# Kernel optimization log

Measured on AMD Instinct MI355X. Metric: run time of the kernel, lower is better.

Reference implementation:

```python
import jax, jax.numpy as jnp
import numpy as np

B, I, S, H, O = 128, 64, 2048, 128, 64


def setup_inputs() -> dict:
    key = jax.random.key(0)
    ks = jax.random.split(key, 9)
    sc = 0.1
    return {
        "x": jax.random.normal(ks[0], (B, I, S), dtype=jnp.float32),
        "Wx_out": jax.random.normal(ks[1], (I, 4 * H), dtype=jnp.float32) * sc,
        "Wh_out": jax.random.normal(ks[2], (H, 4 * H), dtype=jnp.float32) * sc,
        "b_out": jnp.zeros((4 * H,), dtype=jnp.float32),
        "Wx_in": jax.random.normal(ks[3], (H, 4 * H), dtype=jnp.float32) * sc,
        "Wh_in": jax.random.normal(ks[4], (H, 4 * H), dtype=jnp.float32) * sc,
        "b_in": jnp.zeros((4 * H,), dtype=jnp.float32),
        "W_lin": jax.random.normal(ks[5], (O, H), dtype=jnp.float32) * 0.01,
        "b_lin": jnp.zeros((O,), dtype=jnp.float32),
    }


def reference(x, Wx_out, Wh_out, b_out, Wx_in, Wh_in, b_in, W_lin, b_lin):
    # x: (B, I, S) -> permute(0,2,1) -> (B, S, I); scan over time axis.
    xs = jnp.transpose(x, (2, 0, 1))  # (S, B, I)
    h0 = jnp.zeros((x.shape[0], Wh_out.shape[0]), dtype=x.dtype)

    def step(carry, xt):
        h, c, cn = carry  # outer hidden, outer cell, inner cell
        gates = xt @ Wx_out + h @ Wh_out + b_out
        i, f, o, g = jnp.split(gates, 4, axis=-1)
        i, f, o = jax.nn.sigmoid(i), jax.nn.sigmoid(f), jax.nn.sigmoid(o)
        g = jnp.tanh(g)
        x_in = i * g          # inner LSTM input
        h_in = f * c          # inner LSTM hidden
        gi = x_in @ Wx_in + h_in @ Wh_in + b_in
        ii, fi, oi, gg = jnp.split(gi, 4, axis=-1)
        cn_new = jax.nn.sigmoid(fi) * cn + jax.nn.sigmoid(ii) * jnp.tanh(gg)
        c_new = jax.nn.sigmoid(oi) * jnp.tanh(cn_new)  # outer cell = inner hidden
        h_new = o * jnp.tanh(c_new)
        return (h_new, c_new, cn_new), h_new

    _, hs = jax.lax.scan(step, (h0, h0, h0), xs)  # hs: (S, B, H)
    hs = jnp.transpose(hs, (1, 0, 2))             # (B, S, H)
    return hs @ W_lin.T + b_lin                   # (B, S, O)
```

## Files before the change

kernel.cpp:

```cpp
#include <hip/hip_runtime.h>
#include <hip/hip_fp16.h>

#define BB 128
#define II 64
#define SS 2048
#define HH 128
#define GG 512
#define OO 64

typedef _Float16 f16x2 __attribute__((ext_vector_type(2)));
union F4H { float4 f4; f16x2 h[4]; };

__device__ __forceinline__ f16x2 pack2(float a, float b) {
    f16x2 r; r.x = (_Float16)a; r.y = (_Float16)b; return r;
}

__device__ __forceinline__ float dot2(f16x2 w, f16x2 v, float c) {
#if __has_builtin(__builtin_amdgcn_fdot2)
    return __builtin_amdgcn_fdot2(w, v, c, false);
#else
    return fmaf((float)w.x, (float)v.x, fmaf((float)w.y, (float)v.y, c));
#endif
}

__device__ __forceinline__ float tanh_f(float v) {
    float a = fabsf(v);
    float e = __expf(-2.0f * a);
    float r = (1.0f - e) * __builtin_amdgcn_rcpf(1.0f + e);
    return v < 0.0f ? -r : r;
}

template<int P>
__device__ __forceinline__ float qp(float v) {
    return __int_as_float(__builtin_amdgcn_mov_dpp(
        __float_as_int(v), P, 0xF, 0xF, true));
}
template<int C>
__device__ __forceinline__ float qb(float v) { return qp<0x55 * C>(v); }
template<int N>
__device__ __forceinline__ float rolN(float v) {
    return __int_as_float(__builtin_amdgcn_mov_dpp(
        __float_as_int(v), 0x120 + (16 - N), 0xF, 0xF, true));
}

__device__ __forceinline__ void barrier_lds() {
    asm volatile("s_waitcnt lgkmcnt(0)\n\ts_barrier" ::: "memory");
}

__global__ void __launch_bounds__(512)
nlstm_gatex(const float* __restrict__ x, const float* __restrict__ Wx_out,
            const float* __restrict__ b_out, float* __restrict__ gx,
            int t0, int nchunk)
{
    const int bb  = blockIdx.x / nchunk;
    const int tcw = blockIdx.x % nchunk;
    const int j   = threadIdx.x;
    const int u = j >> 2, g = j & 3;
    const int jcol = g * HH + u;

    __shared__ __align__(16) f16x2 xs[128][36];

    f16x2 wxo[II / 2];
#pragma unroll
    for (int m = 0; m < II / 2; ++m)
        wxo[m] = pack2(Wx_out[(2 * m) * GG + jcol],
                       Wx_out[(2 * m + 1) * GG + jcol]);
    const float bo = b_out[jcol];

    const float* xrow = x + (size_t)bb * II * SS;
    const int T0 = t0 + tcw * 128;
#pragma unroll
    for (int r = 0; r < 8; ++r) {
        const int idx = r * 512 + j;
        const int m = idx >> 7, tt = idx & 127;
        xs[tt][m] = pack2(xrow[(size_t)(2 * m) * SS + T0 + tt],
                          xrow[(size_t)(2 * m + 1) * SS + T0 + tt]);
    }
    __syncthreads();

#pragma unroll 1
    for (int tt = 0; tt < 128; ++tt) {
        const float4* xc4 = (const float4*)&xs[tt][0];
        float a0 = bo, a1 = 0.f, a2 = 0.f, a3 = 0.f;
#pragma unroll
        for (int c = 0; c < 8; ++c) {
            F4H xu; xu.f4 = xc4[c];
            a0 = dot2(wxo[4 * c + 0], xu.h[0], a0);
            a1 = dot2(wxo[4 * c + 1], xu.h[1], a1);
            a2 = dot2(wxo[4 * c + 2], xu.h[2], a2);
            a3 = dot2(wxo[4 * c + 3], xu.h[3], a3);
        }
        const float v = (a0 + a1) + (a2 + a3);
        const size_t tl = (size_t)tcw * 128 + tt;
        gx[((size_t)bb * nchunk * 128 + tl) * GG + j] = v;
    }
}

template<bool PROJ_IN>
__global__ void __launch_bounds__(512)
__attribute__((amdgpu_waves_per_eu(2)))
nlstm_scan_seg(
    const float* __restrict__ Wh_out,
    const float* __restrict__ Wx_in, const float* __restrict__ Wh_in,
    const float* __restrict__ b_in,
    const float* __restrict__ W_lin, const float* __restrict__ b_lin,
    const float* __restrict__ gx, float* __restrict__ out,
    f16x2* __restrict__ hws, f16x2* __restrict__ hst,
    float* __restrict__ cst, float* __restrict__ cnst,
    int t0, int t1, int Tc)
{
    const int b = blockIdx.x;
    const int j = threadIdx.x;
    const int u = j >> 2;
    const int g = j & 3;
    const int jcol = g * HH + u;

    __shared__ __align__(16) f16x2 hb[HH / 2];
    __shared__ __align__(16) f16x2 xib[HH / 2];
    __shared__ __align__(16) f16x2 hib[HH / 2];

    f16x2 who[4][16];
    f16x2 wxi[4][16];
    f16x2 whi[4][16];
#pragma unroll
    for (int c = 0; c < 4; ++c)
#pragma unroll
        for (int c4 = 0; c4 < 4; ++c4)
#pragma unroll
            for (int e = 0; e < 4; ++e) {
                const int k0 = 8 * (g + 4 * c4) + 2 * e;
                const int cc = c * HH + u;
                who[c][4 * c4 + e] = pack2(Wh_out[(size_t)k0 * GG + cc],
                                           Wh_out[(size_t)(k0 + 1) * GG + cc]);
                wxi[c][4 * c4 + e] = pack2(Wx_in[(size_t)k0 * GG + cc],
                                           Wx_in[(size_t)(k0 + 1) * GG + cc]);
                whi[c][4 * c4 + e] = pack2(Wh_in[(size_t)k0 * GG + cc],
                                           Wh_in[(size_t)(k0 + 1) * GG + cc]);
            }

    const float bi2 = b_in[jcol];

    const int   pn = j >> 3;
    const int   ps = j & 7;
    float bl = 0.f;
    F4H wl[2];
    if constexpr (PROJ_IN) {
        bl = b_lin[pn];
#pragma unroll
        for (int q = 0; q < 2; ++q) {
            const int c = 2 * ps + q;
#pragma unroll
            for (int r = 0; r < 4; ++r)
                wl[q].h[r] = pack2(W_lin[pn * HH + 8 * c + 2 * r],
                                   W_lin[pn * HH + 8 * c + 2 * r + 1]);
        }
    }

    float* orow = out + (size_t)b * SS * OO;
    f16x2* hrow = (PROJ_IN ? (f16x2*)nullptr : hws + (size_t)b * SS * (HH / 2));
    const float* gxrow = gx + (size_t)b * Tc * GG;

    float c_reg, cn_reg;
    if (t0 == 0) {
        if (j < HH / 2) hb[j] = pack2(0.f, 0.f);
        c_reg = 0.f; cn_reg = 0.f;
    } else {
        if (j < HH / 2) hb[j] = hst[b * (HH / 2) + j];
        c_reg  = cst[b * HH + u];
        cn_reg = cnst[b * HH + u];
    }
    __syncthreads();

    const float4* hb4 = (const float4*)hb;
    const float4* xi4 = (const float4*)xib;
    const float4* hi4 = (const float4*)hib;
    const bool isT = (g == 3);

    float gx_cur = gxrow[j];

#pragma unroll 1
    for (int t = t0; t < t1; ++t) {
        const int tl = t - t0;

        const int tln = (tl + 1 < Tc) ? tl + 1 : tl;
        const float gx_nxt = gxrow[(size_t)tln * GG + j];

        float p0 = 0.f, p1 = 0.f, p2 = 0.f, p3 = 0.f;
#pragma unroll
        for (int c4 = 0; c4 < 4; ++c4) {
            F4H hu; hu.f4 = hb4[g + 4 * c4];
#pragma unroll
            for (int e = 0; e < 4; ++e) {
                p0 = dot2(who[0][4 * c4 + e], hu.h[e], p0);
                p1 = dot2(who[1][4 * c4 + e], hu.h[e], p1);
                p2 = dot2(who[2][4 * c4 + e], hu.h[e], p2);
                p3 = dot2(who[3][4 * c4 + e], hu.h[e], p3);
            }
        }
        p0 += qp<0xB1>(p0); p1 += qp<0xB1>(p1);
        p2 += qp<0xB1>(p2); p3 += qp<0xB1>(p3);
        p0 += qp<0x4E>(p0); p1 += qp<0x4E>(p1);
        p2 += qp<0x4E>(p2); p3 += qp<0x4E>(p3);
        const float totO = (g & 1) ? ((g & 2) ? p3 : p1)
                                   : ((g & 2) ? p2 : p0);
        float acc = totO + gx_cur;

        float ap = isT ? 2.f * acc : acc;
        float s  = __builtin_amdgcn_rcpf(1.f + __expf(-ap));
        float av = isT ? fmaf(2.f, s, -1.f) : s;

        float vi = qb<0>(av), vf = qb<1>(av), vo = qb<2>(av), vg = qb<3>(av);
        float x_in    = vi * vg;
        float h_in    = vf * c_reg;
        float o_outer = vo;

        if constexpr (PROJ_IN) {
            float q0 = 0.f, q1 = 0.f;
            F4H hu0; hu0.f4 = hb4[2 * ps];
            F4H hu1; hu1.f4 = hb4[2 * ps + 1];
            q0 = dot2(wl[0].h[0], hu0.h[0], q0);
            q1 = dot2(wl[0].h[1], hu0.h[1], q1);
            q0 = dot2(wl[0].h[2], hu0.h[2], q0);
            q1 = dot2(wl[0].h[3], hu0.h[3], q1);
            q0 = dot2(wl[1].h[0], hu1.h[0], q0);
            q1 = dot2(wl[1].h[1], hu1.h[1], q1);
            q0 = dot2(wl[1].h[2], hu1.h[2], q0);
            q1 = dot2(wl[1].h[3], hu1.h[3], q1);
            float p = q0 + q1;
            p += rolN<4>(p);
            p += rolN<2>(p);
            p += rolN<1>(p);
            if (ps == 0 && t > 0) orow[(size_t)(t - 1) * OO + pn] = p + bl;
        }

        float xin_n = rolN<4>(x_in);
        float hin_n = rolN<4>(h_in);
        if ((j & 7) == 0) {
            xib[u >> 1] = pack2(x_in, xin_n);
            hib[u >> 1] = pack2(h_in, hin_n);
        }
        barrier_lds();

        float s0 = 0.f, s1 = 0.f, s2 = 0.f, s3 = 0.f;
#pragma unroll
        for (int c4 = 0; c4 < 4; ++c4) {
            F4H xu; xu.f4 = xi4[g + 4 * c4];
#pragma unroll
            for (int e = 0; e < 4; ++e) {
                s0 = dot2(wxi[0][4 * c4 + e], xu.h[e], s0);
                s1 = dot2(wxi[1][4 * c4 + e], xu.h[e], s1);
                s2 = dot2(wxi[2][4 * c4 + e], xu.h[e], s2);
                s3 = dot2(wxi[3][4 * c4 + e], xu.h[e], s3);
            }
        }
#pragma unroll
        for (int c4 = 0; c4 < 4; ++c4) {
            F4H hu2; hu2.f4 = hi4[g + 4 * c4];
#pragma unroll
            for (int e = 0; e < 4; ++e) {
                s0 = dot2(whi[0][4 * c4 + e], hu2.h[e], s0);
                s1 = dot2(whi[1][4 * c4 + e], hu2.h[e], s1);
                s2 = dot2(whi[2][4 * c4 + e], hu2.h[e], s2);
                s3 = dot2(whi[3][4 * c4 + e], hu2.h[e], s3);
            }
        }
        s0 += qp<0xB1>(s0); s1 += qp<0xB1>(s1);
        s2 += qp<0xB1>(s2); s3 += qp<0xB1>(s3);
        s0 += qp<0x4E>(s0); s1 += qp<0x4E>(s1);
        s2 += qp<0x4E>(s2); s3 += qp<0x4E>(s3);
        const float totI = (g & 1) ? ((g & 2) ? s3 : s1)
                                   : ((g & 2) ? s2 : s0);
        float acc2 = totI + bi2;

        float ap2 = isT ? 2.f * acc2 : acc2;
        float s2a = __builtin_amdgcn_rcpf(1.f + __expf(-ap2));
        float av2 = isT ? fmaf(2.f, s2a, -1.f) : s2a;

        float ii = qb<0>(av2), fi = qb<1>(av2), oi = qb<2>(av2), gg = qb<3>(av2);
        float cn_new = fmaf(fi, cn_reg, ii * gg);
        cn_reg = cn_new;
        float c_new = oi * tanh_f(cn_new);
        c_reg = c_new;
        float h_new = o_outer * tanh_f(c_new);

        float hn_n = rolN<4>(h_new);
        if ((j & 7) == 0) {
            f16x2 hp = pack2(h_new, hn_n);
            hb[u >> 1] = hp;
            if constexpr (!PROJ_IN)
                hrow[(size_t)t * (HH / 2) + (j >> 3)] = hp;
        }
        gx_cur = gx_nxt;
        barrier_lds();
    }

    if (j < HH / 2) hst[b * (HH / 2) + j] = hb[j];
    if (g == 0) { cst[b * HH + u] = c_reg; cnst[b * HH + u] = cn_reg; }

    if constexpr (PROJ_IN) {
        if (t1 == SS) {
            float q0 = 0.f, q1 = 0.f;
            F4H hu0; hu0.f4 = hb4[2 * ps];
            F4H hu1; hu1.f4 = hb4[2 * ps + 1];
            q0 = dot2(wl[0].h[0], hu0.h[0], q0);
            q1 = dot2(wl[0].h[1], hu0.h[1], q1);
            q0 = dot2(wl[0].h[2], hu0.h[2], q0);
            q1 = dot2(wl[0].h[3], hu0.h[3], q1);
            q0 = dot2(wl[1].h[0], hu1.h[0], q0);
            q1 = dot2(wl[1].h[1], hu1.h[1], q1);
            q0 = dot2(wl[1].h[2], hu1.h[2], q0);
            q1 = dot2(wl[1].h[3], hu1.h[3], q1);
            float p = q0 + q1;
            p += rolN<4>(p);
            p += rolN<2>(p);
            p += rolN<1>(p);
            if (ps == 0) orow[(size_t)(SS - 1) * OO + pn] = p + bl;
        }
    }
}

__global__ void __launch_bounds__(512)
__attribute__((amdgpu_waves_per_eu(2)))
nlstm_fused(
    const float* __restrict__ x,
    const float* __restrict__ Wx_out, const float* __restrict__ Wh_out,
    const float* __restrict__ b_out,
    const float* __restrict__ Wx_in, const float* __restrict__ Wh_in,
    const float* __restrict__ b_in,
    const float* __restrict__ W_lin, const float* __restrict__ b_lin,
    float* __restrict__ out)
{
    const int b = blockIdx.x;
    const int j = threadIdx.x;
    const int u = j >> 2, g = j & 3;
    const int jcol = g * HH + u;

    __shared__ __align__(16) float4 wxf[8 * 512];
    __shared__ __align__(16) f16x2 xt[2][16][36];
    __shared__ __align__(16) f16x2 hb[HH / 2];
    __shared__ __align__(16) f16x2 xib[HH / 2];
    __shared__ __align__(16) f16x2 hib[HH / 2];

    f16x2 who[HH / 2], wxi[HH / 2], whi[HH / 2];
#pragma unroll
    for (int m = 0; m < HH / 2; ++m)
        who[m] = pack2(Wh_out[(2 * m) * GG + jcol], Wh_out[(2 * m + 1) * GG + jcol]);
#pragma unroll
    for (int m = 0; m < HH / 2; ++m)
        wxi[m] = pack2(Wx_in[(2 * m) * GG + jcol], Wx_in[(2 * m + 1) * GG + jcol]);
#pragma unroll
    for (int m = 0; m < HH / 2; ++m)
        whi[m] = pack2(Wh_in[(2 * m) * GG + jcol], Wh_in[(2 * m + 1) * GG + jcol]);

    const float bo = b_out[jcol];
    const float bi2 = b_in[jcol];
    const int pn = j >> 3, ps = j & 7;
    const float bl = b_lin[pn];
    F4H wl[2];
#pragma unroll
    for (int q = 0; q < 2; ++q) {
        const int c = 2 * ps + q;
#pragma unroll
        for (int r = 0; r < 4; ++r)
            wl[q].h[r] = pack2(W_lin[pn * HH + 8 * c + 2 * r],
                               W_lin[pn * HH + 8 * c + 2 * r + 1]);
    }
#pragma unroll
    for (int c = 0; c < 8; ++c) {
        F4H w4;
#pragma unroll
        for (int q = 0; q < 4; ++q)
            w4.h[q] = pack2(Wx_out[(8 * c + 2 * q) * GG + jcol],
                            Wx_out[(8 * c + 2 * q + 1) * GG + jcol]);
        wxf[c * 512 + j] = w4.f4;
    }

    const float* xrow = x + (size_t)b * II * SS;
    float* orow = out + (size_t)b * SS * OO;
    const int xm = j >> 4, xtl = j & 15;
    const float* xg0 = xrow + (size_t)(2 * xm) * SS + xtl;
    const float* xg1 = xrow + (size_t)(2 * xm + 1) * SS + xtl;

    xt[0][xtl][xm] = pack2(xg0[0], xg1[0]);
    if (j < HH / 2) hb[j] = pack2(0.f, 0.f);
    __syncthreads();

    float c_reg = 0.f, cn_reg = 0.f;
    const float4* hb4 = (const float4*)hb;
    const float4* xi4 = (const float4*)xib;
    const float4* hi4 = (const float4*)hib;
    const bool isT = (g == 3);
    float pr0 = 0.f, pr1 = 0.f;

#pragma unroll 1
    for (int t = 0; t < SS; ++t) {
        const int stl = t & 15;
        const int tb = (t >> 4) & 1;
        if (stl == 0) {
            const int Tn = (t + 16 < SS) ? t + 16 : t;
            pr0 = xg0[Tn];
            pr1 = xg1[Tn];
        }
        const float4* xc4 = (const float4*)&xt[tb][stl][0];
        float a0 = bo, a1 = 0.f, a2 = 0.f, a3 = 0.f;
#pragma unroll
        for (int c = 0; c < 8; ++c) {
            F4H xu; xu.f4 = xc4[c];
            F4H wu; wu.f4 = wxf[c * 512 + j];
            a0 = dot2(wu.h[0], xu.h[0], a0);
            a1 = dot2(wu.h[1], xu.h[1], a1);
            a2 = dot2(wu.h[2], xu.h[2], a2);
            a3 = dot2(wu.h[3], xu.h[3], a3);
        }
#pragma unroll
        for (int c = 0; c < 16; ++c) {
            F4H hu; hu.f4 = hb4[c];
            a0 = dot2(who[4 * c + 0], hu.h[0], a0);
            a1 = dot2(who[4 * c + 1], hu.h[1], a1);
            a2 = dot2(who[4 * c + 2], hu.h[2], a2);
            a3 = dot2(who[4 * c + 3], hu.h[3], a3);
        }
        float acc = (a0 + a1) + (a2 + a3);
        float ap = isT ? 2.f * acc : acc;
        float s = __builtin_amdgcn_rcpf(1.f + __expf(-ap));
        float av = isT ? fmaf(2.f, s, -1.f) : s;
        float vi = qb<0>(av), vf = qb<1>(av), vo = qb<2>(av), vg = qb<3>(av);
        float x_in = vi * vg, h_in = vf * c_reg, o_outer = vo;

        float p0 = 0.f, p1 = 0.f;
        {
            F4H hu0; hu0.f4 = hb4[2 * ps];
            F4H hu1; hu1.f4 = hb4[2 * ps + 1];
            p0 = dot2(wl[0].h[0], hu0.h[0], p0);
            p1 = dot2(wl[0].h[1], hu0.h[1], p1);
            p0 = dot2(wl[0].h[2], hu0.h[2], p0);
            p1 = dot2(wl[0].h[3], hu0.h[3], p1);
            p0 = dot2(wl[1].h[0], hu1.h[0], p0);
            p1 = dot2(wl[1].h[1], hu1.h[1], p1);
            p0 = dot2(wl[1].h[2], hu1.h[2], p0);
            p1 = dot2(wl[1].h[3], hu1.h[3], p1);
        }
        float p = p0 + p1;
        p += rolN<4>(p);
        p += rolN<2>(p);
        p += rolN<1>(p);
        if (ps == 0 && t > 0) orow[(size_t)(t - 1) * OO + pn] = p + bl;

        float xin_n = rolN<4>(x_in);
        float hin_n = rolN<4>(h_in);
        if ((j & 7) == 0) {
            xib[u >> 1] = pack2(x_in, xin_n);
            hib[u >> 1] = pack2(h_in, hin_n);
        }
        barrier_lds();

        float b0 = 0.f, b1 = 0.f, b2 = 0.f, b3 = 0.f;
#pragma unroll
        for (int c = 0; c < 16; ++c) {
            F4H xu; xu.f4 = xi4[c];
            b0 = dot2(wxi[4 * c + 0], xu.h[0], b0);
            b1 = dot2(wxi[4 * c + 1], xu.h[1], b1);
            b2 = dot2(wxi[4 * c + 2], xu.h[2], b2);
            b3 = dot2(wxi[4 * c + 3], xu.h[3], b3);
        }
#pragma unroll
        for (int c = 0; c < 16; ++c) {
            F4H hu; hu.f4 = hi4[c];
            b0 = dot2(whi[4 * c + 0], hu.h[0], b0);
            b1 = dot2(whi[4 * c + 1], hu.h[1], b1);
            b2 = dot2(whi[4 * c + 2], hu.h[2], b2);
            b3 = dot2(whi[4 * c + 3], hu.h[3], b3);
        }
        float acc2 = ((b0 + b1) + (b2 + b3)) + bi2;
        float ap2 = isT ? 2.f * acc2 : acc2;
        float s2 = __builtin_amdgcn_rcpf(1.f + __expf(-ap2));
        float av2 = isT ? fmaf(2.f, s2, -1.f) : s2;
        float ii = qb<0>(av2), fi = qb<1>(av2), oi = qb<2>(av2), gg = qb<3>(av2);
        float cn_new = fmaf(fi, cn_reg, ii * gg);
        cn_reg = cn_new;
        float c_new = oi * tanh_f(cn_new);
        c_reg = c_new;
        float h_new = o_outer * tanh_f(c_new);
        float hn_n = rolN<4>(h_new);
        if ((j & 7) == 0) hb[u >> 1] = pack2(h_new, hn_n);
        if (stl == 0) xt[tb ^ 1][xtl][xm] = pack2(pr0, pr1);
        barrier_lds();
    }
    {
        float p0 = 0.f, p1 = 0.f;
        F4H hu0; hu0.f4 = hb4[2 * ps];
        F4H hu1; hu1.f4 = hb4[2 * ps + 1];
        p0 = dot2(wl[0].h[0], hu0.h[0], p0);
        p1 = dot2(wl[0].h[1], hu0.h[1], p1);
        p0 = dot2(wl[0].h[2], hu0.h[2], p0);
        p1 = dot2(wl[0].h[3], hu0.h[3], p1);
        p0 = dot2(wl[1].h[0], hu1.h[0], p0);
        p1 = dot2(wl[1].h[1], hu1.h[1], p1);
        p0 = dot2(wl[1].h[2], hu1.h[2], p0);
        p1 = dot2(wl[1].h[3], hu1.h[3], p1);
        float p = p0 + p1;
        p += rolN<4>(p);
        p += rolN<2>(p);
        p += rolN<1>(p);
        if (ps == 0) orow[(size_t)(SS - 1) * OO + pn] = p + bl;
    }
}

__global__ void __launch_bounds__(256)
nlstm_proj(const f16x2* __restrict__ hws, const float* __restrict__ W_lin,
           const float* __restrict__ b_lin, float* __restrict__ out)
{
    const int n  = threadIdx.x & 63;
    const int rg = threadIdx.x >> 6;

    f16x2 wn[HH / 2];
#pragma unroll
    for (int k = 0; k < HH / 2; ++k)
        wn[k] = pack2(W_lin[n * HH + 2 * k], W_lin[n * HH + 2 * k + 1]);
    const float bl = b_lin[n];

    const size_t r0 = (size_t)blockIdx.x * 512 + (size_t)rg * 128;
#pragma unroll 1
    for (int rr = 0; rr < 128; ++rr) {
        const size_t r = r0 + rr;
        const float4* hr = (const float4*)(hws + r * (HH / 2));
        float p0 = 0.f, p1 = 0.f, p2 = 0.f, p3 = 0.f;
#pragma unroll
        for (int c = 0; c < 16; ++c) {
            F4H hu; hu.f4 = hr[c];
            p0 = dot2(wn[4 * c + 0], hu.h[0], p0);
            p1 = dot2(wn[4 * c + 1], hu.h[1], p1);
            p2 = dot2(wn[4 * c + 2], hu.h[2], p2);
            p3 = dot2(wn[4 * c + 3], hu.h[3], p3);
        }
        out[r * OO + n] = ((p0 + p1) + (p2 + p3)) + bl;
    }
}

extern "C" void kernel_launch(void* const* d_in, const int* in_sizes, int n_in,
                              void* d_out, int out_size, void* d_ws, size_t ws_size,
                              hipStream_t stream) {
    (void)in_sizes; (void)n_in; (void)out_size;
    const float* x      = (const float*)d_in[0];
    const float* Wx_out = (const float*)d_in[1];
    const float* Wh_out = (const float*)d_in[2];
    const float* b_out  = (const float*)d_in[3];
    const float* Wx_in  = (const float*)d_in[4];
    const float* Wh_in  = (const float*)d_in[5];
    const float* b_in   = (const float*)d_in[6];
    const float* W_lin  = (const float*)d_in[7];
    const float* b_lin  = (const float*)d_in[8];
    float* out = (float*)d_out;

    const size_t hws_b = (size_t)BB * SS * (HH / 2) * sizeof(f16x2);
    const size_t hst_b = (size_t)BB * (HH / 2) * sizeof(f16x2);
    const size_t cst_b = (size_t)BB * HH * sizeof(float);
    const int tcs[5] = {2048, 1024, 512, 256, 128};

    int Tc = 0;
    bool proj_out = false;
    if (d_ws != nullptr) {
        for (int i = 0; i < 5 && Tc == 0; ++i) {
            const size_t gxb = (size_t)BB * tcs[i] * GG * sizeof(float);
            if (ws_size >= hws_b + hst_b + 2 * cst_b + gxb) { Tc = tcs[i]; proj_out = true; }
        }
        for (int i = 0; i < 5 && Tc == 0; ++i) {
            const size_t gxb = (size_t)BB * tcs[i] * GG * sizeof(float);
            if (ws_size >= hst_b + 2 * cst_b + gxb) Tc = tcs[i];
        }
    }

    if (Tc != 0) {
        char* p = (char*)d_ws;
        f16x2* hws = nullptr;
        if (proj_out) { hws = (f16x2*)p; p += hws_b; }
        f16x2* hst = (f16x2*)p; p += hst_b;
        float* cst  = (float*)p; p += cst_b;
        float* cnst = (float*)p; p += cst_b;
        float* gx   = (float*)p;
        const int nchunk = Tc / 128;

        for (int t0 = 0; t0 < SS; t0 += Tc) {
            nlstm_gatex<<<dim3(BB * nchunk), dim3(512), 0, stream>>>(
                x, Wx_out, b_out, gx, t0, nchunk);
            if (proj_out)
                nlstm_scan_seg<false><<<dim3(BB), dim3(512), 0, stream>>>(
                    Wh_out, Wx_in, Wh_in, b_in, W_lin, b_lin, gx, out,
                    hws, hst, cst, cnst, t0, t0 + Tc, Tc);
            else
                nlstm_scan_seg<true><<<dim3(BB), dim3(512), 0, stream>>>(
                    Wh_out, Wx_in, Wh_in, b_in, W_lin, b_lin, gx, out,
                    nullptr, hst, cst, cnst, t0, t0 + Tc, Tc);
        }
        if (proj_out)
            nlstm_proj<<<dim3(512), dim3(256), 0, stream>>>(hws, W_lin, b_lin, out);
    } else {
        nlstm_fused<<<dim3(BB), dim3(512), 0, stream>>>(
            x, Wx_out, Wh_out, b_out, Wx_in, Wh_in, b_in, W_lin, b_lin, out);
    }
}
```

Before: 3.577 ms.

## Fuse input-gate producer and recurrent scan via flag-synchronized ring buffer

Replaces the separate gate-precompute kernel and segmented scan launches with one kernel of 2*BB blocks. Half the blocks produce the x@Wx_out gate chunks into a 3-slot ring buffer and the other half consume them in the recurrence, synchronized through acquire/release flags in global memory. This is meant to overlap gate precompute with the serial scan, cut launch count and gx workspace size, and drop the hidden/cell state save and restore between segments. It relies on producer and consumer blocks being co-resident to avoid deadlock. The projection kernel grid is also doubled with fewer rows per block.

```diff
diff --git a/kernel.cpp b/kernel.cpp
--- a/kernel.cpp
+++ b/kernel.cpp
@@ -7,6 +7,9 @@
 #define HH 128
 #define GG 512
 #define OO 64
+#define CHS 128
+#define NCH (SS / CHS)
+#define RING 3
 
 typedef _Float16 f16x2 __attribute__((ext_vector_type(2)));
 union F4H { float4 f4; f16x2 h[4]; };
@@ -47,77 +50,92 @@
     asm volatile("s_waitcnt lgkmcnt(0)\n\ts_barrier" ::: "memory");
 }
 
-__global__ void __launch_bounds__(512)
-nlstm_gatex(const float* __restrict__ x, const float* __restrict__ Wx_out,
-            const float* __restrict__ b_out, float* __restrict__ gx,
-            int t0, int nchunk)
-{
-    const int bb  = blockIdx.x / nchunk;
-    const int tcw = blockIdx.x % nchunk;
-    const int j   = threadIdx.x;
-    const int u = j >> 2, g = j & 3;
-    const int jcol = g * HH + u;
-
-    __shared__ __align__(16) f16x2 xs[128][36];
-
-    f16x2 wxo[II / 2];
-#pragma unroll
-    for (int m = 0; m < II / 2; ++m)
-        wxo[m] = pack2(Wx_out[(2 * m) * GG + jcol],
-                       Wx_out[(2 * m + 1) * GG + jcol]);
-    const float bo = b_out[jcol];
-
-    const float* xrow = x + (size_t)bb * II * SS;
-    const int T0 = t0 + tcw * 128;
-#pragma unroll
-    for (int r = 0; r < 8; ++r) {
-        const int idx = r * 512 + j;
-        const int m = idx >> 7, tt = idx & 127;
-        xs[tt][m] = pack2(xrow[(size_t)(2 * m) * SS + T0 + tt],
-                          xrow[(size_t)(2 * m + 1) * SS + T0 + tt]);
-    }
-    __syncthreads();
-
-#pragma unroll 1
-    for (int tt = 0; tt < 128; ++tt) {
-        const float4* xc4 = (const float4*)&xs[tt][0];
-        float a0 = bo, a1 = 0.f, a2 = 0.f, a3 = 0.f;
-#pragma unroll
-        for (int c = 0; c < 8; ++c) {
-            F4H xu; xu.f4 = xc4[c];
-            a0 = dot2(wxo[4 * c + 0], xu.h[0], a0);
-            a1 = dot2(wxo[4 * c + 1], xu.h[1], a1);
-            a2 = dot2(wxo[4 * c + 2], xu.h[2], a2);
-            a3 = dot2(wxo[4 * c + 3], xu.h[3], a3);
-        }
-        const float v = (a0 + a1) + (a2 + a3);
-        const size_t tl = (size_t)tcw * 128 + tt;
-        gx[((size_t)bb * nchunk * 128 + tl) * GG + j] = v;
-    }
+__device__ __forceinline__ unsigned ld_acq(const unsigned* p) {
+    return __hip_atomic_load(p, __ATOMIC_ACQUIRE, __HIP_MEMORY_SCOPE_AGENT);
+}
+__device__ __forceinline__ void st_rel(unsigned* p, unsigned v) {
+    __hip_atomic_store(p, v, __ATOMIC_RELEASE, __HIP_MEMORY_SCOPE_AGENT);
 }
 
 template<bool PROJ_IN>
 __global__ void __launch_bounds__(512)
 __attribute__((amdgpu_waves_per_eu(2)))
-nlstm_scan_seg(
-    const float* __restrict__ Wh_out,
+nlstm_fusedpc(
+    const float* __restrict__ x,
+    const float* __restrict__ Wx_out, const float* __restrict__ Wh_out,
+    const float* __restrict__ b_out,
     const float* __restrict__ Wx_in, const float* __restrict__ Wh_in,
     const float* __restrict__ b_in,
     const float* __restrict__ W_lin, const float* __restrict__ b_lin,
-    const float* __restrict__ gx, float* __restrict__ out,
-    f16x2* __restrict__ hws, f16x2* __restrict__ hst,
-    float* __restrict__ cst, float* __restrict__ cnst,
-    int t0, int t1, int Tc)
+    float* __restrict__ out, f16x2* __restrict__ hws,
+    float* __restrict__ gx, unsigned* __restrict__ flag,
+    unsigned* __restrict__ consumed)
 {
-    const int b = blockIdx.x;
+    const int bid = blockIdx.x;
     const int j = threadIdx.x;
     const int u = j >> 2;
     const int g = j & 3;
     const int jcol = g * HH + u;
 
+    __shared__ __align__(16) f16x2 xs[CHS][36];
     __shared__ __align__(16) f16x2 hb[HH / 2];
     __shared__ __align__(16) f16x2 xib[HH / 2];
     __shared__ __align__(16) f16x2 hib[HH / 2];
+
+    if (bid >= BB) {
+        const int bp = bid - BB;
+        f16x2 wxo[II / 2];
+#pragma unroll
+        for (int m = 0; m < II / 2; ++m)
+            wxo[m] = pack2(Wx_out[(2 * m) * GG + jcol],
+                           Wx_out[(2 * m + 1) * GG + jcol]);
+        const float bo = b_out[jcol];
+
+        const float* xrow = x + (size_t)bp * II * SS;
+        float* gxb = gx + (size_t)bp * (RING * CHS) * GG;
+        unsigned* myflag = flag + bp * NCH;
+        unsigned* mycons = consumed + bp * NCH;
+
+        int slot = 0;
+#pragma unroll 1
+        for (int k = 0; k < NCH; ++k) {
+            if (k >= RING) {
+                if (j == 0)
+                    while (ld_acq(&mycons[k - RING]) == 0)
+                        __builtin_amdgcn_s_sleep(2);
+                __syncthreads();
+            }
+            const int T0 = k * CHS;
+#pragma unroll
+            for (int r = 0; r < 8; ++r) {
+                const int idx = r * 512 + j;
+                const int m = idx >> 7, tt = idx & 127;
+                xs[tt][m] = pack2(xrow[(size_t)(2 * m) * SS + T0 + tt],
+                                  xrow[(size_t)(2 * m + 1) * SS + T0 + tt]);
+            }
+            __syncthreads();
+#pragma unroll 1
+            for (int tt = 0; tt < CHS; ++tt) {
+                const float4* xc4 = (const float4*)&xs[tt][0];
+                float a0 = bo, a1 = 0.f, a2 = 0.f, a3 = 0.f;
+#pragma unroll
+                for (int c = 0; c < 8; ++c) {
+                    F4H xu; xu.f4 = xc4[c];
+                    a0 = dot2(wxo[4 * c + 0], xu.h[0], a0);
+                    a1 = dot2(wxo[4 * c + 1], xu.h[1], a1);
+                    a2 = dot2(wxo[4 * c + 2], xu.h[2], a2);
+                    a3 = dot2(wxo[4 * c + 3], xu.h[3], a3);
+                }
+                gxb[(size_t)(slot * CHS + tt) * GG + j] = (a0 + a1) + (a2 + a3);
+            }
+            __syncthreads();
+            if (j == 0) st_rel(&myflag[k], 1u);
+            slot = (slot == RING - 1) ? 0 : slot + 1;
+        }
+        return;
+    }
+
+    const int b = bid;
 
     f16x2 who[4][16];
     f16x2 wxi[4][16];
@@ -158,17 +176,12 @@
 
     float* orow = out + (size_t)b * SS * OO;
     f16x2* hrow = (PROJ_IN ? (f16x2*)nullptr : hws + (size_t)b * SS * (HH / 2));
-    const float* gxrow = gx + (size_t)b * Tc * GG;
-
-    float c_reg, cn_reg;
-    if (t0 == 0) {
-        if (j < HH / 2) hb[j] = pack2(0.f, 0.f);
-        c_reg = 0.f; cn_reg = 0.f;
-    } else {
-        if (j < HH / 2) hb[j] = hst[b * (HH / 2) + j];
-        c_reg  = cst[b * HH + u];
-        cn_reg = cnst[b * HH + u];
-    }
+    const float* gxb = gx + (size_t)b * (RING * CHS) * GG;
+    const unsigned* myflag = flag + b * NCH;
+    unsigned* mycons = consumed + b * NCH;
+
+    if (j < HH / 2) hb[j] = pack2(0.f, 0.f);
+    float c_reg = 0.f, cn_reg = 0.f;
     __syncthreads();
 
     const float4* hb4 = (const float4*)hb;
@@ -176,14 +189,30 @@
     const float4* hi4 = (const float4*)hib;
     const bool isT = (g == 3);
 
-    float gx_cur = gxrow[j];
+    float gx_cur = 0.f;
+    int slot = 0;
 
 #pragma unroll 1
-    for (int t = t0; t < t1; ++t) {
-        const int tl = t - t0;
-
-        const int tln = (tl + 1 < Tc) ? tl + 1 : tl;
-        const float gx_nxt = gxrow[(size_t)tln * GG + j];
+    for (int t = 0; t < SS; ++t) {
+        const int tl7 = t & (CHS - 1);
+
+        if (tl7 == 0) {
+            const int chunk = t >> 7;
+            if (t > 0) {
+                __syncthreads();
+                if (j == 0) st_rel(&mycons[chunk - 1], 1u);
+                slot = (slot == RING - 1) ? 0 : slot + 1;
+            }
+            if (j == 0)
+                while (ld_acq(&myflag[chunk]) == 0)
+                    __builtin_amdgcn_s_sleep(2);
+            __syncthreads();
+            gx_cur = gxb[(size_t)(slot * CHS) * GG + j];
+        }
+
+        float gx_nxt = gx_cur;
+        if (tl7 != CHS - 1)
+            gx_nxt = gxb[(size_t)(slot * CHS + tl7 + 1) * GG + j];
 
         float p0 = 0.f, p1 = 0.f, p2 = 0.f, p3 = 0.f;
 #pragma unroll
@@ -294,28 +323,23 @@
         barrier_lds();
     }
 
-    if (j < HH / 2) hst[b * (HH / 2) + j] = hb[j];
-    if (g == 0) { cst[b * HH + u] = c_reg; cnst[b * HH + u] = cn_reg; }
-
     if constexpr (PROJ_IN) {
-        if (t1 == SS) {
-            float q0 = 0.f, q1 = 0.f;
-            F4H hu0; hu0.f4 = hb4[2 * ps];
-            F4H hu1; hu1.f4 = hb4[2 * ps + 1];
-            q0 = dot2(wl[0].h[0], hu0.h[0], q0);
-            q1 = dot2(wl[0].h[1], hu0.h[1], q1);
-            q0 = dot2(wl[0].h[2], hu0.h[2], q0);
-            q1 = dot2(wl[0].h[3], hu0.h[3], q1);
-            q0 = dot2(wl[1].h[0], hu1.h[0], q0);
-            q1 = dot2(wl[1].h[1], hu1.h[1], q1);
-            q0 = dot2(wl[1].h[2], hu1.h[2], q0);
-            q1 = dot2(wl[1].h[3], hu1.h[3], q1);
-            float p = q0 + q1;
-            p += rolN<4>(p);
-            p += rolN<2>(p);
-            p += rolN<1>(p);
-            if (ps == 0) orow[(size_t)(SS - 1) * OO + pn] = p + bl;
-        }
+        float q0 = 0.f, q1 = 0.f;
+        F4H hu0; hu0.f4 = hb4[2 * ps];
+        F4H hu1; hu1.f4 = hb4[2 * ps + 1];
+        q0 = dot2(wl[0].h[0], hu0.h[0], q0);
+        q1 = dot2(wl[0].h[1], hu0.h[1], q1);
+        q0 = dot2(wl[0].h[2], hu0.h[2], q0);
+        q1 = dot2(wl[0].h[3], hu0.h[3], q1);
+        q0 = dot2(wl[1].h[0], hu1.h[0], q0);
+        q1 = dot2(wl[1].h[1], hu1.h[1], q1);
+        q0 = dot2(wl[1].h[2], hu1.h[2], q0);
+        q1 = dot2(wl[1].h[3], hu1.h[3], q1);
+        float p = q0 + q1;
+        p += rolN<4>(p);
+        p += rolN<2>(p);
+        p += rolN<1>(p);
+        if (ps == 0) orow[(size_t)(SS - 1) * OO + pn] = p + bl;
     }
 }
 
@@ -519,9 +543,9 @@
         wn[k] = pack2(W_lin[n * HH + 2 * k], W_lin[n * HH + 2 * k + 1]);
     const float bl = b_lin[n];
 
-    const size_t r0 = (size_t)blockIdx.x * 512 + (size_t)rg * 128;
+    const size_t r0 = (size_t)blockIdx.x * 256 + (size_t)rg * 64;
 #pragma unroll 1
-    for (int rr = 0; rr < 128; ++rr) {
+    for (int rr = 0; rr < 64; ++rr) {
         const size_t r = r0 + rr;
         const float4* hr = (const float4*)(hws + r * (HH / 2));
         float p0 = 0.f, p1 = 0.f, p2 = 0.f, p3 = 0.f;
@@ -552,48 +576,36 @@
     const float* b_lin  = (const float*)d_in[8];
     float* out = (float*)d_out;
 
-    const size_t hws_b = (size_t)BB * SS * (HH / 2) * sizeof(f16x2);
-    const size_t hst_b = (size_t)BB * (HH / 2) * sizeof(f16x2);
-    const size_t cst_b = (size_t)BB * HH * sizeof(float);
-    const int tcs[5] = {2048, 1024, 512, 256, 128};
-
-    int Tc = 0;
-    bool proj_out = false;
-    if (d_ws != nullptr) {
-        for (int i = 0; i < 5 && Tc == 0; ++i) {
-            const size_t gxb = (size_t)BB * tcs[i] * GG * sizeof(float);
-            if (ws_size >= hws_b + hst_b + 2 * cst_b + gxb) { Tc = tcs[i]; proj_out = true; }
-        }
-        for (int i = 0; i < 5 && Tc == 0; ++i) {
-            const size_t gxb = (size_t)BB * tcs[i] * GG * sizeof(float);
-            if (ws_size >= hst_b + 2 * cst_b + gxb) Tc = tcs[i];
-        }
-    }
-
-    if (Tc != 0) {
+    const size_t hws_b  = (size_t)BB * SS * (HH / 2) * sizeof(f16x2);
+    const size_t flg_b  = (size_t)BB * NCH * sizeof(unsigned);
+    const size_t ring_b = (size_t)BB * RING * CHS * GG * sizeof(float);
+    const size_t need_full = hws_b + 2 * flg_b + ring_b;
+    const size_t need_min  = 2 * flg_b + ring_b;
+
+    if (d_ws != nullptr && ws_size >= need_full) {
         char* p = (char*)d_ws;
-        f16x2* hws = nullptr;
-        if (proj_out) { hws = (f16x2*)p; p += hws_b; }
-        f16x2* hst = (f16x2*)p; p += hst_b;
-        float* cst  = (float*)p; p += cst_b;
-        float* cnst = (float*)p; p += cst_b;
-        float* gx   = (float*)p;
-        const int nchunk = Tc / 128;
-
-        for (int t0 = 0; t0 < SS; t0 += Tc) {
-            nlstm_gatex<<<dim3(BB * nchunk), dim3(512), 0, stream>>>(
-                x, Wx_out, b_out, gx, t0, nchunk);
-            if (proj_out)
-                nlstm_scan_seg<false><<<dim3(BB), dim3(512), 0, stream>>>(
-                    Wh_out, Wx_in, Wh_in, b_in, W_lin, b_lin, gx, out,
-                    hws, hst, cst, cnst, t0, t0 + Tc, Tc);
-            else
-                nlstm_scan_seg<true><<<dim3(BB), dim3(512), 0, stream>>>(
-                    Wh_out, Wx_in, Wh_in, b_in, W_lin, b_lin, gx, out,
-                    nullptr, hst, cst, cnst, t0, t0 + Tc, Tc);
-        }
-        if (proj_out)
-            nlstm_proj<<<dim3(512), dim3(256), 0, stream>>>(hws, W_lin, b_lin, out);
+        f16x2* hws = (f16x2*)p;          p += hws_b;
+        unsigned* flags = (unsigned*)p;  p += 2 * flg_b;
+        float* gx = (float*)p;
+        unsigned* flag = flags;
+        unsigned* consumed = flags + BB * NCH;
+
+        hipMemsetAsync(flags, 0, 2 * flg_b, stream);
+        nlstm_fusedpc<false><<<dim3(2 * BB), dim3(512), 0, stream>>>(
+            x, Wx_out, Wh_out, b_out, Wx_in, Wh_in, b_in, W_lin, b_lin,
+            out, hws, gx, flag, consumed);
+        nlstm_proj<<<dim3(1024), dim3(256), 0, stream>>>(hws, W_lin, b_lin, out);
+    } else if (d_ws != nullptr && ws_size >= need_min) {
+        char* p = (char*)d_ws;
+        unsigned* flags = (unsigned*)p;  p += 2 * flg_b;
+        float* gx = (float*)p;
+        unsigned* flag = flags;
+        unsigned* consumed = flags + BB * NCH;
+
+        hipMemsetAsync(flags, 0, 2 * flg_b, stream);
+        nlstm_fusedpc<true><<<dim3(2 * BB), dim3(512), 0, stream>>>(
+            x, Wx_out, Wh_out, b_out, Wx_in, Wh_in, b_in, W_lin, b_lin,
+            out, nullptr, gx, flag, consumed);
     } else {
         nlstm_fused<<<dim3(BB), dim3(512), 0, stream>>>(
             x, Wx_out, Wh_out, b_out, Wx_in, Wh_in, b_in, W_lin, b_lin, out);
```

Measured after the change: 3.838 ms. 7.3% more time.
